# Kernel optimization log

Hardware: AMD Instinct MI355X
Metric: run time of the kernel (lower is better)

The kernel has to match this reference:

```python
import jax, jax.numpy as jnp
import numpy as np

N = 100000      # nodes
E = 1600000     # edges (avg degree 16)
D = 128         # feature dim (in_dim == out_dim)
ALPHA = 0.1     # initial-residual mixing
BETA = 0.5      # identity-mapping / linear mixing


def setup_inputs() -> dict:
    key = jax.random.key(0)
    k1, k2, k3, k4, k5 = jax.random.split(key, 5)
    features = jax.random.normal(k1, (N, D), dtype=jnp.float32)
    initial_features = jax.random.normal(k2, (N, D), dtype=jnp.float32)
    # xavier_uniform with relu gain sqrt(2): bound = gain * sqrt(6/(fan_in+fan_out))
    bound = np.sqrt(2.0) * np.sqrt(6.0 / (D + D))
    W = jax.random.uniform(k5, (D, D), dtype=jnp.float32, minval=-bound, maxval=bound)
    src = jax.random.randint(k3, (E,), 0, N, dtype=jnp.int32)
    dst = jax.random.randint(k4, (E,), 0, N, dtype=jnp.int32)
    return {"features": features, "initial_features": initial_features,
            "W": W, "src": src, "dst": dst}


def reference(features, initial_features, W, src, dst):
    # symmetric degree normalization (edge weights are all ones)
    degs = jax.ops.segment_sum(jnp.ones((E,), features.dtype), dst, num_segments=N)
    norm = jnp.power(jnp.maximum(degs, 1.0), -0.5)[:, None]          # [N,1]
    h = features * norm                                               # [N,D]
    # message passing: m_e = h[src_e] * w_e (w=1); aggregate sum into dst
    agg = jax.ops.segment_sum(h[src], dst, num_segments=N)            # [N,D]
    h = agg * norm
    # alpha initial-residual, beta identity-mapped linear combine
    h = (1.0 - ALPHA) * h + ALPHA * initial_features
    h = (1.0 - BETA) * h + BETA * (h @ W.T)
    return jax.nn.relu(h)
```

## Files before the change

### kernel.cpp

```cpp
#include <hip/hip_runtime.h>
#include <math.h>

#define D 128
#define THREADS 256
#define BS 512
#define MAXB 1024
#define CAP 9216
#define BIN_T 512
#define EPT 4
#define BIN_CHUNK (BIN_T * EPT)

typedef __attribute__((ext_vector_type(8))) short s16x8;
typedef __attribute__((ext_vector_type(4))) float f32x4;
typedef __attribute__((ext_vector_type(4))) float f4;
typedef __attribute__((ext_vector_type(4))) unsigned u4;

__device__ __forceinline__ unsigned short f2bf(float f) {
    unsigned u = __float_as_uint(f);
    u += 0x7FFFu + ((u >> 16) & 1u);
    return (unsigned short)(u >> 16);
}
__device__ __forceinline__ float bflo(unsigned u) { return __uint_as_float(u << 16); }
__device__ __forceinline__ float bfhi(unsigned u) { return __uint_as_float(u & 0xFFFF0000u); }

__global__ __launch_bounds__(THREADS) void k_init(int* __restrict__ bcur,
                                                  int* __restrict__ ocnt, int nbuck) {
    const int b = blockIdx.x * THREADS + threadIdx.x;
    if (b < nbuck) bcur[b] = b * CAP;
    if (b == 0) *ocnt = 0;
}

__global__ __launch_bounds__(BIN_T) void k_bin(const int* __restrict__ src,
                                               const int* __restrict__ dst,
                                               int* __restrict__ bcur,
                                               unsigned* __restrict__ ebuf,
                                               int2* __restrict__ ovf,
                                               int* __restrict__ ocnt,
                                               int E, int nbuck) {
    __shared__ int lh[2 * MAXB];
    __shared__ int lbase[2 * MAXB];
    const int tid = threadIdx.x;
    const int sub = tid & 1;
    for (int b = tid; b < 2 * nbuck; b += BIN_T) lh[b] = 0;
    __syncthreads();
    const int e0 = blockIdx.x * BIN_CHUNK + tid * EPT;
    int bk[EPT];
    unsigned pk[EPT];
    if (e0 + EPT <= E) {
        const int4 d4 = *reinterpret_cast<const int4*>(dst + e0);
        const int4 s4 = *reinterpret_cast<const int4*>(src + e0);
        const int dd[4] = {d4.x, d4.y, d4.z, d4.w};
        const int ss[4] = {s4.x, s4.y, s4.z, s4.w};
#pragma unroll
        for (int k = 0; k < EPT; ++k) {
            bk[k] = dd[k] >> 9;
            pk[k] = ((unsigned)ss[k] << 9) | (unsigned)(dd[k] & (BS - 1));
            atomicAdd(&lh[bk[k] * 2 + sub], 1);
        }
    } else {
#pragma unroll
        for (int k = 0; k < EPT; ++k) {
            const int e = e0 + k;
            if (e < E) {
                const int d = dst[e];
                bk[k] = d >> 9;
                pk[k] = ((unsigned)src[e] << 9) | (unsigned)(d & (BS - 1));
                atomicAdd(&lh[bk[k] * 2 + sub], 1);
            } else {
                bk[k] = -1;
            }
        }
    }
    __syncthreads();
    for (int b = tid; b < nbuck; b += BIN_T) {
        const int c0 = lh[b * 2], c1 = lh[b * 2 + 1];
        const int v = c0 + c1;
        const int base = v ? atomicAdd(&bcur[b], v) : 0;
        lbase[b * 2] = base;
        lbase[b * 2 + 1] = base + c0;
        lh[b * 2] = 0;
        lh[b * 2 + 1] = 0;
    }
    __syncthreads();
#pragma unroll
    for (int k = 0; k < EPT; ++k) {
        if (bk[k] >= 0) {
            const int slot = bk[k] * 2 + sub;
            const int pos = lbase[slot] + atomicAdd(&lh[slot], 1);
            if (pos < (bk[k] + 1) * CAP) {
                ebuf[pos] = pk[k];
            } else {
                const int op = atomicAdd(ocnt, 1);
                ovf[op] = make_int2((int)pk[k], bk[k]);
            }
        }
    }
}

__global__ __launch_bounds__(BS) void k_csr(const unsigned* __restrict__ ebuf,
                                            const int* __restrict__ bcur,
                                            const int2* __restrict__ ovf,
                                            const int* __restrict__ ocnt,
                                            int* __restrict__ csr,
                                            int2* __restrict__ offdeg,
                                            float* __restrict__ normf,
                                            int n, int nbuck) {
    __shared__ unsigned sedge[CAP];
    __shared__ int cnt[BS];
    __shared__ int ex[BS];
    const int b = blockIdx.x, tid = threadIdx.x;
    const int lo = b * CAP;
    const int m = min(bcur[b], lo + CAP) - lo;
    const int oc = *ocnt;
    cnt[tid] = 0;
    __syncthreads();
    for (int i = tid; i < m; i += BS) {
        const unsigned pe = ebuf[lo + i];
        sedge[i] = pe;
        atomicAdd(&cnt[pe & (BS - 1)], 1);
    }
    for (int i = tid; i < oc; i += BS) {
        const int2 o = ovf[i];
        if (o.y == b) atomicAdd(&cnt[(unsigned)o.x & (BS - 1)], 1);
    }
    __syncthreads();
    const int deg = cnt[tid];
    ex[tid] = deg;
    __syncthreads();
    for (int s = 1; s < BS; s <<= 1) {
        const int t = (tid >= s) ? ex[tid - s] : 0;
        __syncthreads();
        ex[tid] += t;
        __syncthreads();
    }
    const int excl = ex[tid] - deg;
    const int node = b * BS + tid;
    if (node < n) {
        offdeg[node] = make_int2(lo + excl, deg);
        normf[node] = rsqrtf(fmaxf((float)deg, 1.0f));
    }
    cnt[tid] = excl;
    __syncthreads();
    const int csrEnd = nbuck * CAP;
    for (int i = tid; i < m; i += BS) {
        const unsigned pe = sedge[i];
        const int p = atomicAdd(&cnt[pe & (BS - 1)], 1);
        if (lo + p < csrEnd) csr[lo + p] = (int)(pe >> 9);
    }
    for (int i = tid; i < oc; i += BS) {
        const int2 o = ovf[i];
        if (o.y == b) {
            const unsigned pe = (unsigned)o.x;
            const int p = atomicAdd(&cnt[pe & (BS - 1)], 1);
            if (lo + p < csrEnd) csr[lo + p] = (int)(pe >> 9);
        }
    }
}

__global__ __launch_bounds__(THREADS) void k_scale(
    const float* __restrict__ f, const float* __restrict__ nrm,
    uint4* __restrict__ hb, int n) {
    int c = blockIdx.x * THREADS + threadIdx.x;
    if (c >= n * 16) return;
    float nv = nrm[c >> 4];
    const f4* fp = (const f4*)f;
    const f4 a = __builtin_nontemporal_load(fp + c * 2);
    const f4 b = __builtin_nontemporal_load(fp + c * 2 + 1);
    uint4 o;
    o.x = f2bf(a.x * nv) | ((unsigned)f2bf(a.y * nv) << 16);
    o.y = f2bf(a.z * nv) | ((unsigned)f2bf(a.w * nv) << 16);
    o.z = f2bf(b.x * nv) | ((unsigned)f2bf(b.y * nv) << 16);
    o.w = f2bf(b.z * nv) | ((unsigned)f2bf(b.w * nv) << 16);
    hb[c] = o;
}

__global__ __launch_bounds__(THREADS) void k_gather_csr(
    const uint4* __restrict__ hb, const float* __restrict__ initf,
    const int2* __restrict__ offdeg, const int* __restrict__ csr,
    const float* __restrict__ normf, uint4* __restrict__ tb, int n) {
    const int g = (blockIdx.x * THREADS + threadIdx.x) >> 4;
    if (g >= n) return;
    const int gl = threadIdx.x & 15;

    float acc[8] = {0.f, 0.f, 0.f, 0.f, 0.f, 0.f, 0.f, 0.f};

#define ROW(S)                                                      \
    {                                                               \
        const uint4 r = hb[(size_t)(S)*16 + gl];                    \
        acc[0] += bflo(r.x); acc[1] += bfhi(r.x);                   \
        acc[2] += bflo(r.y); acc[3] += bfhi(r.y);                   \
        acc[4] += bflo(r.z); acc[5] += bfhi(r.z);                   \
        acc[6] += bflo(r.w); acc[7] += bfhi(r.w);                   \
    }
    const int2 od = offdeg[g];
    const int begin = od.x, end = od.x + od.y;
    int j = begin;
    for (; j + 8 <= end; j += 8) {
        const int4 a4 = *reinterpret_cast<const int4*>(csr + j);
        const int4 b4 = *reinterpret_cast<const int4*>(csr + j + 4);
        ROW(a4.x); ROW(a4.y); ROW(a4.z); ROW(a4.w);
        ROW(b4.x); ROW(b4.y); ROW(b4.z); ROW(b4.w);
    }
    for (; j + 4 <= end; j += 4) {
        const int4 a4 = *reinterpret_cast<const int4*>(csr + j);
        ROW(a4.x); ROW(a4.y); ROW(a4.z); ROW(a4.w);
    }
    for (; j < end; ++j) ROW(csr[j]);
#undef ROW

    const float nv = 0.9f * normf[g];
    const f4* iv = (const f4*)(initf + (size_t)g * D);
    const f4 i0 = __builtin_nontemporal_load(iv + gl * 2);
    const f4 i1 = __builtin_nontemporal_load(iv + gl * 2 + 1);
    float t[8];
    t[0] = nv * acc[0] + 0.1f * i0.x; t[1] = nv * acc[1] + 0.1f * i0.y;
    t[2] = nv * acc[2] + 0.1f * i0.z; t[3] = nv * acc[3] + 0.1f * i0.w;
    t[4] = nv * acc[4] + 0.1f * i1.x; t[5] = nv * acc[5] + 0.1f * i1.y;
    t[6] = nv * acc[6] + 0.1f * i1.z; t[7] = nv * acc[7] + 0.1f * i1.w;
    u4 o;
    o.x = f2bf(t[0]) | ((unsigned)f2bf(t[1]) << 16);
    o.y = f2bf(t[2]) | ((unsigned)f2bf(t[3]) << 16);
    o.z = f2bf(t[4]) | ((unsigned)f2bf(t[5]) << 16);
    o.w = f2bf(t[6]) | ((unsigned)f2bf(t[7]) << 16);
    __builtin_nontemporal_store(o, (u4*)tb + (size_t)g * 16 + gl);
}

__device__ __forceinline__ void stage_M(const float* __restrict__ W,
                                        uint4* __restrict__ sMt, int tid) {
    for (int c = tid; c < D * 16; c += THREADS) {
        const int j = c >> 4, kc = c & 15;
        const float* wr = W + j * D + kc * 8;
        float m[8];
#pragma unroll
        for (int q = 0; q < 8; ++q) m[q] = 0.5f * wr[q];
        const int dj = j - kc * 8;
        if (dj >= 0 && dj < 8) m[dj] += 0.5f;
        uint4 o;
        o.x = f2bf(m[0]) | ((unsigned)f2bf(m[1]) << 16);
        o.y = f2bf(m[2]) | ((unsigned)f2bf(m[3]) << 16);
        o.z = f2bf(m[4]) | ((unsigned)f2bf(m[5]) << 16);
        o.w = f2bf(m[6]) | ((unsigned)f2bf(m[7]) << 16);
        sMt[j * 16 + (kc ^ (j & 7))] = o;
    }
}

__device__ __forceinline__ void gemm_tile(const uint4* __restrict__ sMt,
                                          const uint4* __restrict__ sT,
                                          float* __restrict__ out,
                                          int base, int n, int lane, int wave) {
    const int l15 = lane & 15, lq = lane >> 4;
    const int mt = wave & 1, ntb = (wave >> 1) * 4;
    const int nr = mt * 16 + l15;
    s16x8 a[4];
#pragma unroll
    for (int ks = 0; ks < 4; ++ks)
        a[ks] = *reinterpret_cast<const s16x8*>(
            &sT[nr * 16 + ((ks * 4 + lq) ^ (nr & 7))]);

#pragma unroll
    for (int tnt = 0; tnt < 4; ++tnt) {
        const int nt = ntb + tnt;
        const int jr = nt * 16 + l15;
        f32x4 c = {0.f, 0.f, 0.f, 0.f};
#pragma unroll
        for (int ks = 0; ks < 4; ++ks) {
            const s16x8 b = *reinterpret_cast<const s16x8*>(
                &sMt[jr * 16 + ((ks * 4 + lq) ^ (jr & 7))]);
            c = __builtin_amdgcn_mfma_f32_16x16x32_bf16(a[ks], b, c, 0, 0, 0);
        }
        const int col = nt * 16 + l15;
        const int row0 = base + mt * 16 + lq * 4;
#pragma unroll
        for (int r = 0; r < 4; ++r) {
            const int node = row0 + r;
            if (node < n)
                __builtin_nontemporal_store(fmaxf(c[r], 0.f),
                                            &out[(size_t)node * D + col]);
        }
    }
}

__global__ __launch_bounds__(THREADS) void k_gemm_tb(
    const float* __restrict__ W, const uint4* __restrict__ tb,
    float* __restrict__ out, int n, int numTiles) {
    __shared__ uint4 sMt[D * 16];
    __shared__ uint4 sT[32 * 16];
    const int tid = threadIdx.x;
    stage_M(W, sMt, tid);
    __syncthreads();

    const int sn = tid >> 3;
    const int c0 = (tid & 7) * 2;
    const int wave = tid >> 6, lane = tid & 63;

    for (int tile = blockIdx.x; tile < numTiles; tile += gridDim.x) {
        const int base = tile << 5;
        {
            const int node = base + sn;
#pragma unroll
            for (int s = 0; s < 2; ++s) {
                const int cc = c0 + s;
                uint4 o;
                if (node < n) {
                    const u4 t = __builtin_nontemporal_load(
                        (const u4*)tb + (size_t)node * 16 + cc);
                    o.x = t.x; o.y = t.y; o.z = t.z; o.w = t.w;
                } else {
                    o.x = o.y = o.z = o.w = 0u;
                }
                sT[sn * 16 + (cc ^ (sn & 7))] = o;
            }
        }
        __syncthreads();
        gemm_tile(sMt, sT, out, base, n, lane, wave);
        __syncthreads();
    }
}

__global__ __launch_bounds__(THREADS) void k_build1(
    const int* __restrict__ src, const int* __restrict__ dst,
    int* __restrict__ head, int2* __restrict__ p, int E) {
    int e = blockIdx.x * THREADS + threadIdx.x;
    if (e < E) {
        int nx = atomicExch(&head[dst[e]], e);
        p[e] = make_int2(nx, src[e]);
    }
}

__global__ __launch_bounds__(THREADS) void k_normwalk1(
    const int* __restrict__ head, const int2* __restrict__ p,
    float* __restrict__ normf, int n) {
    int i = blockIdx.x * THREADS + threadIdx.x;
    if (i >= n) return;
    int c = head[i], cnt = 0;
    while (c >= 0) { ++cnt; c = p[c].x; }
    normf[i] = rsqrtf(fmaxf((float)cnt, 1.0f));
}

__global__ __launch_bounds__(THREADS) void k_gatherchain(
    const float* __restrict__ features, const float* __restrict__ initf,
    const int* __restrict__ head, const int2* __restrict__ p,
    const float* __restrict__ normf, float* __restrict__ out, int n) {
    const int g = (blockIdx.x * THREADS + threadIdx.x) >> 4;
    if (g >= n) return;
    const int gl = threadIdx.x & 15;
    float acc[8] = {0.f, 0.f, 0.f, 0.f, 0.f, 0.f, 0.f, 0.f};
    int c = head[g];
    while (c >= 0) {
        const int2 pc = p[c];
        const float w = normf[pc.y];
        const float4* fr = (const float4*)(features + (size_t)pc.y * D);
        const float4 f0 = fr[gl * 2], f1 = fr[gl * 2 + 1];
        acc[0] += f0.x * w; acc[1] += f0.y * w;
        acc[2] += f0.z * w; acc[3] += f0.w * w;
        acc[4] += f1.x * w; acc[5] += f1.y * w;
        acc[6] += f1.z * w; acc[7] += f1.w * w;
        c = pc.x;
    }
    const float nv = 0.9f * normf[g];
    const float4* iv = (const float4*)(initf + (size_t)g * D);
    const float4 i0 = iv[gl * 2], i1 = iv[gl * 2 + 1];
    float4 t0, t1;
    t0.x = nv * acc[0] + 0.1f * i0.x; t0.y = nv * acc[1] + 0.1f * i0.y;
    t0.z = nv * acc[2] + 0.1f * i0.z; t0.w = nv * acc[3] + 0.1f * i0.w;
    t1.x = nv * acc[4] + 0.1f * i1.x; t1.y = nv * acc[5] + 0.1f * i1.y;
    t1.z = nv * acc[6] + 0.1f * i1.z; t1.w = nv * acc[7] + 0.1f * i1.w;
    float4* orow = (float4*)(out + (size_t)g * D);
    orow[gl * 2] = t0;
    orow[gl * 2 + 1] = t1;
}

__global__ __launch_bounds__(THREADS) void k_gemm_ip(
    const float* __restrict__ W, float* __restrict__ out, int n, int numTiles) {
    __shared__ uint4 sMt[D * 16];
    __shared__ uint4 sT[32 * 16];
    const int tid = threadIdx.x;
    stage_M(W, sMt, tid);
    __syncthreads();
    const int sn = tid >> 3;
    const int c0 = (tid & 7) * 2;
    const int wave = tid >> 6, lane = tid & 63;
    for (int tile = blockIdx.x; tile < numTiles; tile += gridDim.x) {
        const int base = tile << 5;
        {
            const int node = base + sn;
#pragma unroll
            for (int s = 0; s < 2; ++s) {
                const int cc = c0 + s;
                uint4 o;
                if (node < n) {
                    const float4* tr = (const float4*)(out + (size_t)node * D);
                    const float4 a = tr[cc * 2], b = tr[cc * 2 + 1];
                    o.x = f2bf(a.x) | ((unsigned)f2bf(a.y) << 16);
                    o.y = f2bf(a.z) | ((unsigned)f2bf(a.w) << 16);
                    o.z = f2bf(b.x) | ((unsigned)f2bf(b.y) << 16);
                    o.w = f2bf(b.z) | ((unsigned)f2bf(b.w) << 16);
                } else {
                    o.x = o.y = o.z = o.w = 0u;
                }
                sT[sn * 16 + (cc ^ (sn & 7))] = o;
            }
        }
        __syncthreads();
        gemm_tile(sMt, sT, out, base, n, lane, wave);
        __syncthreads();
    }
}

extern "C" void kernel_launch(void* const* d_in, const int* in_sizes, int n_in,
                              void* d_out, int out_size, void* d_ws, size_t ws_size,
                              hipStream_t stream) {
    const float* features = (const float*)d_in[0];
    const float* initf    = (const float*)d_in[1];
    const float* W        = (const float*)d_in[2];
    const int*   src      = (const int*)d_in[3];
    const int*   dst      = (const int*)d_in[4];
    float* out = (float*)d_out;

    const int n = in_sizes[0] / D;
    const int E = in_sizes[3];
    if (n <= 0) return;

    const int nbuck = (n + BS - 1) / BS;
    const int numTiles = (n + 31) >> 5;
    const int gridT = numTiles < 1024 ? numTiles : 1024;
    const int gridG = (int)(((size_t)n * 16 + THREADS - 1) / THREADS);

    const size_t odA  = ((size_t)n * 8 + 15) & ~(size_t)15;
    const size_t nA   = ((size_t)n * 4 + 15) & ~(size_t)15;
    const size_t bA   = ((size_t)MAXB * 4 + 16);
    const size_t slabA = ((size_t)nbuck * CAP * 4 + 15) & ~(size_t)15;
    const size_t hbA  = (size_t)n * 256;
    const size_t tbA  = (size_t)n * 256;
    const size_t needMain = odA + nA + bA + 2 * slabA + hbA + tbA;

    if (nbuck <= MAXB && n <= (1 << 23) && ws_size >= needMain) {
        char* w = (char*)d_ws;
        int2*     offdeg = (int2*)w;              w += odA;
        float*    normf  = (float*)w;             w += nA;
        int*      bcur   = (int*)w;
        int*      ocnt   = (int*)(w + (size_t)MAXB * 4);  w += bA;
        unsigned* ebuf   = (unsigned*)w;          w += slabA;
        int*      csr    = (int*)w;               w += slabA;
        uint4*    hb     = (uint4*)w;             w += hbA;
        uint4*    tb     = (uint4*)w;
        int2*     ovf    = (int2*)tb;

        k_init<<<(nbuck + THREADS - 1) / THREADS, THREADS, 0, stream>>>(bcur, ocnt, nbuck);
        k_bin<<<(E + BIN_CHUNK - 1) / BIN_CHUNK, BIN_T, 0, stream>>>(
            src, dst, bcur, ebuf, ovf, ocnt, E, nbuck);
        k_csr<<<nbuck, BS, 0, stream>>>(ebuf, bcur, ovf, ocnt, csr, offdeg, normf, n, nbuck);
        k_scale<<<(n * 16 + THREADS - 1) / THREADS, THREADS, 0, stream>>>(
            features, normf, hb, n);
        k_gather_csr<<<gridG, THREADS, 0, stream>>>(hb, initf, offdeg, csr, normf, tb, n);
        k_gemm_tb<<<gridT, THREADS, 0, stream>>>(W, tb, out, n, numTiles);
    } else {
        const size_t pA = ((size_t)E * 8 + 15) & ~(size_t)15;
        float* normf = (float*)d_ws;
        int*   head  = (int*)((char*)d_ws + nA);
        int2*  p     = (int2*)((char*)d_ws + 2 * nA);
        if (ws_size < 2 * nA + pA) return;
        hipMemsetAsync(head, 0xFF, (size_t)n * 4, stream);
        k_build1<<<(E + THREADS - 1) / THREADS, THREADS, 0, stream>>>(src, dst, head, p, E);
        k_normwalk1<<<(n + THREADS - 1) / THREADS, THREADS, 0, stream>>>(head, p, normf, n);
        k_gatherchain<<<gridG, THREADS, 0, stream>>>(features, initf, head, p, normf, out, n);
        k_gemm_ip<<<gridT, THREADS, 0, stream>>>(W, out, n, numTiles);
    }
}
```

Before: 173.0 us.

## Move initial-residual add into GEMM staging, simplify binning and CSR build

```diff
diff --git a/kernel.cpp b/kernel.cpp
--- a/kernel.cpp
+++ b/kernel.cpp
@@ -7,7 +7,7 @@
 #define MAXB 1024
 #define CAP 9216
 #define BIN_T 512
-#define EPT 4
+#define EPT 16
 #define BIN_CHUNK (BIN_T * EPT)
 
 typedef __attribute__((ext_vector_type(8))) short s16x8;
@@ -22,13 +22,6 @@
 }
 __device__ __forceinline__ float bflo(unsigned u) { return __uint_as_float(u << 16); }
 __device__ __forceinline__ float bfhi(unsigned u) { return __uint_as_float(u & 0xFFFF0000u); }
-
-__global__ __launch_bounds__(THREADS) void k_init(int* __restrict__ bcur,
-                                                  int* __restrict__ ocnt, int nbuck) {
-    const int b = blockIdx.x * THREADS + threadIdx.x;
-    if (b < nbuck) bcur[b] = b * CAP;
-    if (b == 0) *ocnt = 0;
-}
 
 __global__ __launch_bounds__(BIN_T) void k_bin(const int* __restrict__ src,
                                                const int* __restrict__ dst,
@@ -37,58 +30,39 @@
                                                int2* __restrict__ ovf,
                                                int* __restrict__ ocnt,
                                                int E, int nbuck) {
-    __shared__ int lh[2 * MAXB];
-    __shared__ int lbase[2 * MAXB];
+    __shared__ int lh[MAXB];
+    __shared__ int lbase[MAXB];
     const int tid = threadIdx.x;
-    const int sub = tid & 1;
-    for (int b = tid; b < 2 * nbuck; b += BIN_T) lh[b] = 0;
-    __syncthreads();
-    const int e0 = blockIdx.x * BIN_CHUNK + tid * EPT;
+    for (int b = tid; b < nbuck; b += BIN_T) lh[b] = 0;
+    __syncthreads();
+    const int base = blockIdx.x * BIN_CHUNK;
     int bk[EPT];
     unsigned pk[EPT];
-    if (e0 + EPT <= E) {
-        const int4 d4 = *reinterpret_cast<const int4*>(dst + e0);
-        const int4 s4 = *reinterpret_cast<const int4*>(src + e0);
-        const int dd[4] = {d4.x, d4.y, d4.z, d4.w};
-        const int ss[4] = {s4.x, s4.y, s4.z, s4.w};
-#pragma unroll
-        for (int k = 0; k < EPT; ++k) {
-            bk[k] = dd[k] >> 9;
-            pk[k] = ((unsigned)ss[k] << 9) | (unsigned)(dd[k] & (BS - 1));
-            atomicAdd(&lh[bk[k] * 2 + sub], 1);
-        }
-    } else {
-#pragma unroll
-        for (int k = 0; k < EPT; ++k) {
-            const int e = e0 + k;
-            if (e < E) {
-                const int d = dst[e];
-                bk[k] = d >> 9;
-                pk[k] = ((unsigned)src[e] << 9) | (unsigned)(d & (BS - 1));
-                atomicAdd(&lh[bk[k] * 2 + sub], 1);
-            } else {
-                bk[k] = -1;
-            }
+#pragma unroll
+    for (int k = 0; k < EPT; ++k) {
+        const int e = base + k * BIN_T + tid;
+        if (e < E) {
+            const int d = dst[e];
+            bk[k] = d >> 9;
+            pk[k] = ((unsigned)src[e] << 9) | (unsigned)(d & (BS - 1));
+            atomicAdd(&lh[bk[k]], 1);
+        } else {
+            bk[k] = -1;
         }
     }
     __syncthreads();
     for (int b = tid; b < nbuck; b += BIN_T) {
-        const int c0 = lh[b * 2], c1 = lh[b * 2 + 1];
-        const int v = c0 + c1;
-        const int base = v ? atomicAdd(&bcur[b], v) : 0;
-        lbase[b * 2] = base;
-        lbase[b * 2 + 1] = base + c0;
-        lh[b * 2] = 0;
-        lh[b * 2 + 1] = 0;
+        const int v = lh[b];
+        lbase[b] = v ? atomicAdd(&bcur[b], v) : 0;
+        lh[b] = 0;
     }
     __syncthreads();
 #pragma unroll
     for (int k = 0; k < EPT; ++k) {
         if (bk[k] >= 0) {
-            const int slot = bk[k] * 2 + sub;
-            const int pos = lbase[slot] + atomicAdd(&lh[slot], 1);
-            if (pos < (bk[k] + 1) * CAP) {
-                ebuf[pos] = pk[k];
+            const int r = lbase[bk[k]] + atomicAdd(&lh[bk[k]], 1);
+            if (r < CAP) {
+                ebuf[(size_t)bk[k] * CAP + r] = pk[k];
             } else {
                 const int op = atomicAdd(ocnt, 1);
                 ovf[op] = make_int2((int)pk[k], bk[k]);
@@ -105,20 +79,16 @@
                                             int2* __restrict__ offdeg,
                                             float* __restrict__ normf,
                                             int n, int nbuck) {
-    __shared__ unsigned sedge[CAP];
     __shared__ int cnt[BS];
     __shared__ int ex[BS];
     const int b = blockIdx.x, tid = threadIdx.x;
     const int lo = b * CAP;
-    const int m = min(bcur[b], lo + CAP) - lo;
+    const int m = min(bcur[b], CAP);
     const int oc = *ocnt;
     cnt[tid] = 0;
     __syncthreads();
-    for (int i = tid; i < m; i += BS) {
-        const unsigned pe = ebuf[lo + i];
-        sedge[i] = pe;
-        atomicAdd(&cnt[pe & (BS - 1)], 1);
-    }
+    for (int i = tid; i < m; i += BS)
+        atomicAdd(&cnt[ebuf[lo + i] & (BS - 1)], 1);
     for (int i = tid; i < oc; i += BS) {
         const int2 o = ovf[i];
         if (o.y == b) atomicAdd(&cnt[(unsigned)o.x & (BS - 1)], 1);
@@ -143,7 +113,7 @@
     __syncthreads();
     const int csrEnd = nbuck * CAP;
     for (int i = tid; i < m; i += BS) {
-        const unsigned pe = sedge[i];
+        const unsigned pe = ebuf[lo + i];
         const int p = atomicAdd(&cnt[pe & (BS - 1)], 1);
         if (lo + p < csrEnd) csr[lo + p] = (int)(pe >> 9);
     }
@@ -175,7 +145,7 @@
 }
 
 __global__ __launch_bounds__(THREADS) void k_gather_csr(
-    const uint4* __restrict__ hb, const float* __restrict__ initf,
+    const uint4* __restrict__ hb,
     const int2* __restrict__ offdeg, const int* __restrict__ csr,
     const float* __restrict__ normf, uint4* __restrict__ tb, int n) {
     const int g = (blockIdx.x * THREADS + threadIdx.x) >> 4;
@@ -209,19 +179,11 @@
 #undef ROW
 
     const float nv = 0.9f * normf[g];
-    const f4* iv = (const f4*)(initf + (size_t)g * D);
-    const f4 i0 = __builtin_nontemporal_load(iv + gl * 2);
-    const f4 i1 = __builtin_nontemporal_load(iv + gl * 2 + 1);
-    float t[8];
-    t[0] = nv * acc[0] + 0.1f * i0.x; t[1] = nv * acc[1] + 0.1f * i0.y;
-    t[2] = nv * acc[2] + 0.1f * i0.z; t[3] = nv * acc[3] + 0.1f * i0.w;
-    t[4] = nv * acc[4] + 0.1f * i1.x; t[5] = nv * acc[5] + 0.1f * i1.y;
-    t[6] = nv * acc[6] + 0.1f * i1.z; t[7] = nv * acc[7] + 0.1f * i1.w;
     u4 o;
-    o.x = f2bf(t[0]) | ((unsigned)f2bf(t[1]) << 16);
-    o.y = f2bf(t[2]) | ((unsigned)f2bf(t[3]) << 16);
-    o.z = f2bf(t[4]) | ((unsigned)f2bf(t[5]) << 16);
-    o.w = f2bf(t[6]) | ((unsigned)f2bf(t[7]) << 16);
+    o.x = f2bf(nv * acc[0]) | ((unsigned)f2bf(nv * acc[1]) << 16);
+    o.y = f2bf(nv * acc[2]) | ((unsigned)f2bf(nv * acc[3]) << 16);
+    o.z = f2bf(nv * acc[4]) | ((unsigned)f2bf(nv * acc[5]) << 16);
+    o.w = f2bf(nv * acc[6]) | ((unsigned)f2bf(nv * acc[7]) << 16);
     __builtin_nontemporal_store(o, (u4*)tb + (size_t)g * 16 + gl);
 }
 
@@ -282,7 +244,8 @@
 
 __global__ __launch_bounds__(THREADS) void k_gemm_tb(
     const float* __restrict__ W, const uint4* __restrict__ tb,
-    float* __restrict__ out, int n, int numTiles) {
+    const float* __restrict__ initf, float* __restrict__ out,
+    int n, int numTiles) {
     __shared__ uint4 sMt[D * 16];
     __shared__ uint4 sT[32 * 16];
     const int tid = threadIdx.x;
@@ -304,7 +267,21 @@
                 if (node < n) {
                     const u4 t = __builtin_nontemporal_load(
                         (const u4*)tb + (size_t)node * 16 + cc);
-                    o.x = t.x; o.y = t.y; o.z = t.z; o.w = t.w;
+                    const f4* iv = (const f4*)(initf + (size_t)node * D);
+                    const f4 i0 = __builtin_nontemporal_load(iv + cc * 2);
+                    const f4 i1 = __builtin_nontemporal_load(iv + cc * 2 + 1);
+                    const float v0 = bflo(t.x) + 0.1f * i0.x;
+                    const float v1 = bfhi(t.x) + 0.1f * i0.y;
+                    const float v2 = bflo(t.y) + 0.1f * i0.z;
+                    const float v3 = bfhi(t.y) + 0.1f * i0.w;
+                    const float v4 = bflo(t.z) + 0.1f * i1.x;
+                    const float v5 = bfhi(t.z) + 0.1f * i1.y;
+                    const float v6 = bflo(t.w) + 0.1f * i1.z;
+                    const float v7 = bfhi(t.w) + 0.1f * i1.w;
+                    o.x = f2bf(v0) | ((unsigned)f2bf(v1) << 16);
+                    o.y = f2bf(v2) | ((unsigned)f2bf(v3) << 16);
+                    o.z = f2bf(v4) | ((unsigned)f2bf(v5) << 16);
+                    o.w = f2bf(v6) | ((unsigned)f2bf(v7) << 16);
                 } else {
                     o.x = o.y = o.z = o.w = 0u;
                 }
@@ -446,14 +423,14 @@
         uint4*    tb     = (uint4*)w;
         int2*     ovf    = (int2*)tb;
 
-        k_init<<<(nbuck + THREADS - 1) / THREADS, THREADS, 0, stream>>>(bcur, ocnt, nbuck);
+        hipMemsetAsync(bcur, 0, (size_t)MAXB * 4 + 16, stream);
         k_bin<<<(E + BIN_CHUNK - 1) / BIN_CHUNK, BIN_T, 0, stream>>>(
             src, dst, bcur, ebuf, ovf, ocnt, E, nbuck);
         k_csr<<<nbuck, BS, 0, stream>>>(ebuf, bcur, ovf, ocnt, csr, offdeg, normf, n, nbuck);
         k_scale<<<(n * 16 + THREADS - 1) / THREADS, THREADS, 0, stream>>>(
             features, normf, hb, n);
-        k_gather_csr<<<gridG, THREADS, 0, stream>>>(hb, initf, offdeg, csr, normf, tb, n);
-        k_gemm_tb<<<gridT, THREADS, 0, stream>>>(W, tb, out, n, numTiles);
+        k_gather_csr<<<gridG, THREADS, 0, stream>>>(hb, offdeg, csr, normf, tb, n);
+        k_gemm_tb<<<gridT, THREADS, 0, stream>>>(W, tb, initf, out, n, numTiles);
     } else {
         const size_t pA = ((size_t)E * 8 + 15) & ~(size_t)15;
         float* normf = (float*)d_ws;
```

Result: no change. 171.2 us (-1.0%).
